# Kernel tuning notes

Measured on AMD Instinct MI355X. Metric: run time of the kernel, lower is better.

The kernel has to match this reference:

```python
import jax, jax.numpy as jnp
import numpy as np

# ---- static config (mirrors MonitorRetina init) ----
N, S, H, W = 256, 1, 144, 256        # stimulus: [N, S, H, W]
HR, WR = 144, 256                    # retina height/width
FOV_HALF_RAD = 0.5 * 75.0 * np.pi / 180.0   # Angular retina, degrees=75
GELU_GAMMA = 1.7015043497085571      # variance-preserving gain for gelu
OUT_OF_RANGE = 10.0                  # grid value for rays missing the monitor


def isotropic_grid_2d(h, w):
    """Pixel-center coordinates, isotropic (normalized by max dim), [-1,1] on the long axis."""
    m = float(max(h, w))
    y = (jnp.arange(h, dtype=jnp.float32) * 2.0 + 1.0 - h) / m
    x = (jnp.arange(w, dtype=jnp.float32) * 2.0 + 1.0 - w) / m
    gy, gx = jnp.meshgrid(y, x, indexing="ij")
    return gx, gy  # each [h, w]


def rmat_3d(ax, ay, az):
    """Batched 3D rotation matrix R = Rz @ Ry @ Rx from Euler angles, each [N]."""
    cx, sx = jnp.cos(ax), jnp.sin(ax)
    cy, sy = jnp.cos(ay), jnp.sin(ay)
    cz, sz = jnp.cos(az), jnp.sin(az)
    one, zero = jnp.ones_like(ax), jnp.zeros_like(ax)
    Rx = jnp.stack([one, zero, zero, zero, cx, -sx, zero, sx, cx], -1).reshape(-1, 3, 3)
    Ry = jnp.stack([cy, zero, sy, zero, one, zero, -sy, zero, cy], -1).reshape(-1, 3, 3)
    Rz = jnp.stack([cz, -sz, zero, sz, cz, zero, zero, zero, one], -1).reshape(-1, 3, 3)
    return jnp.einsum("nij,njk,nkl->nil", Rz, Ry, Rx)  # [N,3,3]


def retina_rays(rmat):
    """Angular retina: pixel angles -> unit ray directions, rotated per batch. [N,HR,WR,3]."""
    gx, gy = isotropic_grid_2d(HR, WR)
    ax, ay = gx * FOV_HALF_RAD, gy * FOV_HALF_RAD
    a = jnp.sqrt(ax * ax + ay * ay) + 1e-12
    sinc = jnp.sin(a) / a
    d = jnp.stack([sinc * ax, sinc * ay, jnp.cos(a)], -1)  # [HR,WR,3]
    return jnp.einsum("nij,hwj->nhwi", rmat, d)


def monitor_project(rays):
    """Plane monitor at unit distance along +z: perspective divide to isotropic grid coords. [N,HR,WR,2]."""
    rz = rays[..., 2]
    safe = rz > 1e-3
    inv = jnp.where(safe, rz, 1.0)
    gx = jnp.where(safe, rays[..., 0] / inv, OUT_OF_RANGE)
    gy = jnp.where(safe, rays[..., 1] / inv, OUT_OF_RANGE)
    return jnp.stack([gx, gy], -1)


def isotropic_grid_sample_2d(x, grid, pad_value=0.0):
    """Bilinear sample x:[N,C,H,W] at grid:[N,H',W',2] (isotropic coords), constant padding."""
    m = float(max(H, W))
    px = (grid[..., 0] * m + W - 1.0) * 0.5  # [N,H',W'] pixel coords
    py = (grid[..., 1] * m + H - 1.0) * 0.5
    x0 = jnp.floor(px)
    y0 = jnp.floor(py)
    wx = px - x0
    wy = py - y0
    x0i = x0.astype(jnp.int32)
    y0i = y0.astype(jnp.int32)

    def corner(img, yi, xi):
        valid = (xi >= 0) & (xi < W) & (yi >= 0) & (yi < H)
        v = img[:, jnp.clip(yi, 0, H - 1), jnp.clip(xi, 0, W - 1)]  # [C,H',W']
        return jnp.where(valid[None], v, pad_value)

    def one(img, y0i, x0i, wx, wy):
        v00 = corner(img, y0i, x0i)
        v01 = corner(img, y0i, x0i + 1)
        v10 = corner(img, y0i + 1, x0i)
        v11 = corner(img, y0i + 1, x0i + 1)
        return (v00 * (1 - wx) + v01 * wx) * (1 - wy) + (v10 * (1 - wx) + v11 * wx) * wy

    return jax.vmap(one)(x, y0i, x0i, wx, wy)  # [N,C,H',W']


def setup_inputs() -> dict:
    key = jax.random.key(0)
    ks = jax.random.split(key, 8)
    F, D = 16, 128
    return {
        "stimulus": jax.random.normal(ks[0], (N, S, H, W), jnp.float32),
        "perspective": jax.random.normal(ks[1], (N, F), jnp.float32),
        "W1": jax.random.normal(ks[2], (F, D), jnp.float32) / np.sqrt(F),
        "b1": jnp.zeros((D,), jnp.float32),
        "W2": jax.random.normal(ks[3], (D, D), jnp.float32) / np.sqrt(D),
        "b2": jnp.zeros((D,), jnp.float32),
        "Wp": jax.random.normal(ks[4], (D, 3), jnp.float32) * 0.05,  # proj gains init near 0
        "bp": jnp.zeros((3,), jnp.float32),
    }


def reference(stimulus, perspective, W1, b1, W2, b2, Wp, bp):
    # MLP -> 3 angles -> rotation matrix (rmat)
    h = jax.nn.gelu(perspective @ W1 + b1) * GELU_GAMMA
    h = jax.nn.gelu(h @ W2 + b2) * GELU_GAMMA
    ang = h @ Wp + bp                      # [N,3]
    rm = rmat_3d(ang[:, 0], ang[:, 1], ang[:, 2])
    rays = retina_rays(rm)                 # [N,HR,WR,3]
    grid = monitor_project(rays)           # [N,HR,WR,2]
    # monitor_pixel / retina_pixel are Raw (identity) transforms
    return isotropic_grid_sample_2d(stimulus, grid, pad_value=0.0)  # [N,S,HR,WR]
```

## Files before the change

### kernel.cpp

```cpp
#include <hip/hip_runtime.h>
#include <math.h>

#define NB    256
#define IMG_H 144
#define IMG_W 256
#define HR    144
#define WR    256
#define FDIM  16
#define DDIM  128

#define FOV_HALF_RAD 0.6544984694978736f
#define GELU_GAMMA   1.7015043497085571f
#define OUT_OF_RANGE 10.0f

__device__ __forceinline__ float gelu_gamma(float x) {
    const float k0 = 0.7978845608028654f;
    const float k1 = 0.044715f;
    float t = tanhf(k0 * (x + k1 * x * x * x));
    return 0.5f * x * (1.0f + t) * GELU_GAMMA;
}

__global__ void __launch_bounds__(DDIM) mlp_rmat_kernel(
    const float* __restrict__ persp,
    const float* __restrict__ W1,
    const float* __restrict__ b1,
    const float* __restrict__ W2,
    const float* __restrict__ b2,
    const float* __restrict__ Wp,
    const float* __restrict__ bp,
    float* __restrict__ Rout)
{
    const int n = blockIdx.x;
    const int d = threadIdx.x;

    __shared__ float sh1[DDIM];
    __shared__ float sh2[DDIM];
    __shared__ float ang[3];

    float acc = b1[d];
#pragma unroll
    for (int f = 0; f < FDIM; ++f)
        acc += persp[n * FDIM + f] * W1[f * DDIM + d];
    sh1[d] = gelu_gamma(acc);
    __syncthreads();

    float acc2 = b2[d];
#pragma unroll 8
    for (int k = 0; k < DDIM; ++k)
        acc2 += sh1[k] * W2[k * DDIM + d];
    sh2[d] = gelu_gamma(acc2);
    __syncthreads();

    if (d < 3) {
        float a = bp[d];
#pragma unroll 8
        for (int k = 0; k < DDIM; ++k)
            a += sh2[k] * Wp[k * 3 + d];
        ang[d] = a;
    }
    __syncthreads();

    if (d == 0) {
        float cx = cosf(ang[0]), sx = sinf(ang[0]);
        float cy = cosf(ang[1]), sy = sinf(ang[1]);
        float cz = cosf(ang[2]), sz = sinf(ang[2]);
        float* R = Rout + n * 9;
        R[0] = cz * cy;  R[1] = cz * sy * sx - sz * cx;  R[2] = cz * sy * cx + sz * sx;
        R[3] = sz * cy;  R[4] = sz * sy * sx + cz * cx;  R[5] = sz * sy * cx - cz * sx;
        R[6] = -sy;      R[7] = cy * sx;                 R[8] = cy * cx;
    }
}

__device__ __forceinline__ float fetch_px(const float* __restrict__ img, int yi, int xi) {
    bool valid = (xi >= 0) & (xi < IMG_W) & (yi >= 0) & (yi < IMG_H);
    return valid ? img[yi * IMG_W + xi] : 0.0f;
}

__global__ void __launch_bounds__(WR) retina_sample_kernel(
    const float* __restrict__ stim,
    const float* __restrict__ Rmat,
    float* __restrict__ out)
{
    const int w = threadIdx.x;
    const int h = blockIdx.x;
    const int n = blockIdx.y;

    const float* Rn = Rmat + n * 9;
    const float r0 = Rn[0], r1 = Rn[1], r2 = Rn[2];
    const float r3 = Rn[3], r4 = Rn[4], r5 = Rn[5];
    const float r6 = Rn[6], r7 = Rn[7], r8 = Rn[8];

    const float gx = (2.0f * w + 1.0f - 256.0f) * (1.0f / 256.0f);
    const float gy = (2.0f * h + 1.0f - 144.0f) * (1.0f / 256.0f);

    const float axv = gx * FOV_HALF_RAD;
    const float ayv = gy * FOV_HALF_RAD;
    const float t   = axv * axv + ayv * ayv;

    float sc = fmaf(t, 2.7557319e-6f, -1.9841270e-4f);
    sc = fmaf(t, sc,  8.3333333e-3f);
    sc = fmaf(t, sc, -1.6666667e-1f);
    sc = fmaf(t, sc,  1.0f);

    float ca = fmaf(t, 2.4801587e-5f, -1.3888889e-3f);
    ca = fmaf(t, ca,  4.1666667e-2f);
    ca = fmaf(t, ca, -0.5f);
    ca = fmaf(t, ca,  1.0f);

    const float dx = sc * axv, dy = sc * ayv, dz = ca;

    const float rx = r0 * dx + r1 * dy + r2 * dz;
    const float ry = r3 * dx + r4 * dy + r5 * dz;
    const float rz = r6 * dx + r7 * dy + r8 * dz;

    const float inv = __builtin_amdgcn_rcpf(rz);
    const bool safe = rz > 0.001f;
    const float gxp = safe ? rx * inv : OUT_OF_RANGE;
    const float gyp = safe ? ry * inv : OUT_OF_RANGE;

    const float px = fmaf(gxp, 256.0f, (float)(IMG_W - 1)) * 0.5f;
    const float py = fmaf(gyp, 256.0f, (float)(IMG_H - 1)) * 0.5f;

    const float x0f = floorf(px), y0f = floorf(py);
    const float wx = px - x0f, wy = py - y0f;
    const int x0 = (int)x0f, y0 = (int)y0f;

    const float* __restrict__ img = stim + (size_t)n * (IMG_H * IMG_W);
    const float v00 = fetch_px(img, y0,     x0);
    const float v01 = fetch_px(img, y0,     x0 + 1);
    const float v10 = fetch_px(img, y0 + 1, x0);
    const float v11 = fetch_px(img, y0 + 1, x0 + 1);

    const float top = v00 * (1.0f - wx) + v01 * wx;
    const float bot = v10 * (1.0f - wx) + v11 * wx;
    const float val = top * (1.0f - wy) + bot * wy;

    out[((size_t)n * HR + h) * WR + w] = val;
}

extern "C" void kernel_launch(void* const* d_in, const int* in_sizes, int n_in,
                              void* d_out, int out_size, void* d_ws, size_t ws_size,
                              hipStream_t stream) {
    const float* stimulus    = (const float*)d_in[0];
    const float* perspective = (const float*)d_in[1];
    const float* W1          = (const float*)d_in[2];
    const float* b1          = (const float*)d_in[3];
    const float* W2          = (const float*)d_in[4];
    const float* b2          = (const float*)d_in[5];
    const float* Wp          = (const float*)d_in[6];
    const float* bp          = (const float*)d_in[7];
    float* out = (float*)d_out;

    float* Rmat = (float*)d_ws;

    mlp_rmat_kernel<<<NB, DDIM, 0, stream>>>(
        perspective, W1, b1, W2, b2, Wp, bp, Rmat);

    dim3 grid(HR, NB);
    retina_sample_kernel<<<grid, WR, 0, stream>>>(stimulus, Rmat, out);
}
```

Before: 126.8 us.

## Compute four pixels per thread with vectorized nontemporal stores in retina sampler

Each thread now handles four adjacent output pixels instead of one, and each block covers four rows instead of one. All gather loads are issued together before the interpolation arithmetic, and results are written with a single 128-bit nontemporal store. The goal is more memory-level parallelism per thread, fewer blocks to schedule, fewer store instructions, and less cache pollution from the output stream. In exchange, each gather touches a wider spread of addresses per wavefront, register pressure goes up, and there are fewer threads overall.

```diff
diff --git a/kernel.cpp b/kernel.cpp
--- a/kernel.cpp
+++ b/kernel.cpp
@@ -12,6 +12,8 @@
 #define FOV_HALF_RAD 0.6544984694978736f
 #define GELU_GAMMA   1.7015043497085571f
 #define OUT_OF_RANGE 10.0f
+
+typedef float f32x4 __attribute__((ext_vector_type(4)));
 
 __device__ __forceinline__ float gelu_gamma(float x) {
     const float k0 = 0.7978845608028654f;
@@ -72,70 +74,88 @@
 }
 
 __device__ __forceinline__ float fetch_px(const float* __restrict__ img, int yi, int xi) {
-    bool valid = (xi >= 0) & (xi < IMG_W) & (yi >= 0) & (yi < IMG_H);
+    bool valid = ((unsigned)xi < IMG_W) & ((unsigned)yi < IMG_H);
     return valid ? img[yi * IMG_W + xi] : 0.0f;
 }
 
-__global__ void __launch_bounds__(WR) retina_sample_kernel(
+__global__ void __launch_bounds__(256) retina_sample_kernel(
     const float* __restrict__ stim,
     const float* __restrict__ Rmat,
     float* __restrict__ out)
 {
-    const int w = threadIdx.x;
-    const int h = blockIdx.x;
-    const int n = blockIdx.y;
+    const int tid = threadIdx.x;
+    const int n   = blockIdx.y;
+    const int h   = blockIdx.x * 4 + (tid >> 6);
+    const int w0  = (tid & 63) * 4;
 
     const float* Rn = Rmat + n * 9;
     const float r0 = Rn[0], r1 = Rn[1], r2 = Rn[2];
     const float r3 = Rn[3], r4 = Rn[4], r5 = Rn[5];
     const float r6 = Rn[6], r7 = Rn[7], r8 = Rn[8];
 
-    const float gx = (2.0f * w + 1.0f - 256.0f) * (1.0f / 256.0f);
-    const float gy = (2.0f * h + 1.0f - 144.0f) * (1.0f / 256.0f);
-
-    const float axv = gx * FOV_HALF_RAD;
+    const float gy  = (2.0f * h + 1.0f - 144.0f) * (1.0f / 256.0f);
     const float ayv = gy * FOV_HALF_RAD;
-    const float t   = axv * axv + ayv * ayv;
-
-    float sc = fmaf(t, 2.7557319e-6f, -1.9841270e-4f);
-    sc = fmaf(t, sc,  8.3333333e-3f);
-    sc = fmaf(t, sc, -1.6666667e-1f);
-    sc = fmaf(t, sc,  1.0f);
-
-    float ca = fmaf(t, 2.4801587e-5f, -1.3888889e-3f);
-    ca = fmaf(t, ca,  4.1666667e-2f);
-    ca = fmaf(t, ca, -0.5f);
-    ca = fmaf(t, ca,  1.0f);
-
-    const float dx = sc * axv, dy = sc * ayv, dz = ca;
-
-    const float rx = r0 * dx + r1 * dy + r2 * dz;
-    const float ry = r3 * dx + r4 * dy + r5 * dz;
-    const float rz = r6 * dx + r7 * dy + r8 * dz;
-
-    const float inv = __builtin_amdgcn_rcpf(rz);
-    const bool safe = rz > 0.001f;
-    const float gxp = safe ? rx * inv : OUT_OF_RANGE;
-    const float gyp = safe ? ry * inv : OUT_OF_RANGE;
-
-    const float px = fmaf(gxp, 256.0f, (float)(IMG_W - 1)) * 0.5f;
-    const float py = fmaf(gyp, 256.0f, (float)(IMG_H - 1)) * 0.5f;
-
-    const float x0f = floorf(px), y0f = floorf(py);
-    const float wx = px - x0f, wy = py - y0f;
-    const int x0 = (int)x0f, y0 = (int)y0f;
+    const float ay2 = ayv * ayv;
 
     const float* __restrict__ img = stim + (size_t)n * (IMG_H * IMG_W);
-    const float v00 = fetch_px(img, y0,     x0);
-    const float v01 = fetch_px(img, y0,     x0 + 1);
-    const float v10 = fetch_px(img, y0 + 1, x0);
-    const float v11 = fetch_px(img, y0 + 1, x0 + 1);
 
-    const float top = v00 * (1.0f - wx) + v01 * wx;
-    const float bot = v10 * (1.0f - wx) + v11 * wx;
-    const float val = top * (1.0f - wy) + bot * wy;
+    float px_[4], py_[4];
+    int   x0_[4], y0_[4];
+    float v00[4], v01[4], v10[4], v11[4];
 
-    out[((size_t)n * HR + h) * WR + w] = val;
+#pragma unroll
+    for (int j = 0; j < 4; ++j) {
+        const float gx  = (2.0f * (w0 + j) + 1.0f - 256.0f) * (1.0f / 256.0f);
+        const float axv = gx * FOV_HALF_RAD;
+        const float t   = axv * axv + ay2;
+
+        float sc = fmaf(t, 2.7557319e-6f, -1.9841270e-4f);
+        sc = fmaf(t, sc,  8.3333333e-3f);
+        sc = fmaf(t, sc, -1.6666667e-1f);
+        sc = fmaf(t, sc,  1.0f);
+
+        float ca = fmaf(t, 2.4801587e-5f, -1.3888889e-3f);
+        ca = fmaf(t, ca,  4.1666667e-2f);
+        ca = fmaf(t, ca, -0.5f);
+        ca = fmaf(t, ca,  1.0f);
+
+        const float dx = sc * axv, dy = sc * ayv, dz = ca;
+
+        const float rx = r0 * dx + r1 * dy + r2 * dz;
+        const float ry = r3 * dx + r4 * dy + r5 * dz;
+        const float rz = r6 * dx + r7 * dy + r8 * dz;
+
+        const float inv = __builtin_amdgcn_rcpf(rz);
+        const bool safe = rz > 0.001f;
+        const float gxp = safe ? rx * inv : OUT_OF_RANGE;
+        const float gyp = safe ? ry * inv : OUT_OF_RANGE;
+
+        px_[j] = fmaf(gxp, 256.0f, (float)(IMG_W - 1)) * 0.5f;
+        py_[j] = fmaf(gyp, 256.0f, (float)(IMG_H - 1)) * 0.5f;
+        x0_[j] = (int)floorf(px_[j]);
+        y0_[j] = (int)floorf(py_[j]);
+    }
+
+#pragma unroll
+    for (int j = 0; j < 4; ++j) {
+        v00[j] = fetch_px(img, y0_[j],     x0_[j]);
+        v01[j] = fetch_px(img, y0_[j],     x0_[j] + 1);
+        v10[j] = fetch_px(img, y0_[j] + 1, x0_[j]);
+        v11[j] = fetch_px(img, y0_[j] + 1, x0_[j] + 1);
+    }
+
+    f32x4 res;
+#pragma unroll
+    for (int j = 0; j < 4; ++j) {
+        const float wx = px_[j] - floorf(px_[j]);
+        const float wy = py_[j] - floorf(py_[j]);
+        const float top = v00[j] * (1.0f - wx) + v01[j] * wx;
+        const float bot = v10[j] * (1.0f - wx) + v11[j] * wx;
+        res[j] = top * (1.0f - wy) + bot * wy;
+    }
+
+    f32x4* dst = (f32x4*)(out + ((size_t)n * HR + h) * WR + w0);
+    __builtin_nontemporal_store(res, dst);
 }
 
 extern "C" void kernel_launch(void* const* d_in, const int* in_sizes, int n_in,
@@ -156,6 +176,6 @@
     mlp_rmat_kernel<<<NB, DDIM, 0, stream>>>(
         perspective, W1, b1, W2, b2, Wp, bp, Rmat);
 
-    dim3 grid(HR, NB);
-    retina_sample_kernel<<<grid, WR, 0, stream>>>(stimulus, Rmat, out);
+    dim3 grid(HR / 4, NB);
+    retina_sample_kernel<<<grid, 256, 0, stream>>>(stimulus, Rmat, out);
 }
```

After: 129.9 us. +2.4%, slower.

## Stage whole stimulus image in LDS per block and sample from shared memory

Applied to the files above, without the earlier changes.

Each block now handles one batch item. It copies the full 144x256 image into shared memory with vector loads, then each thread computes four output pixels and gathers their bilinear taps from LDS. Results go out as 128-bit nontemporal stores. This replaces scattered global gathers with LDS reads and reduces the block count. The trade-off is that one block per CU with a large LDS footprint leaves no overlap between the load phase and the compute phase.

```diff
diff --git a/kernel.cpp b/kernel.cpp
--- a/kernel.cpp
+++ b/kernel.cpp
@@ -4,6 +4,7 @@
 #define NB    256
 #define IMG_H 144
 #define IMG_W 256
+#define IMG_ELEMS (IMG_H * IMG_W)
 #define HR    144
 #define WR    256
 #define FDIM  16
@@ -12,6 +13,8 @@
 #define FOV_HALF_RAD 0.6544984694978736f
 #define GELU_GAMMA   1.7015043497085571f
 #define OUT_OF_RANGE 10.0f
+
+typedef float f32x4 __attribute__((ext_vector_type(4)));
 
 __device__ __forceinline__ float gelu_gamma(float x) {
     const float k0 = 0.7978845608028654f;
@@ -71,71 +74,105 @@
     }
 }
 
-__device__ __forceinline__ float fetch_px(const float* __restrict__ img, int yi, int xi) {
-    bool valid = (xi >= 0) & (xi < IMG_W) & (yi >= 0) & (yi < IMG_H);
-    return valid ? img[yi * IMG_W + xi] : 0.0f;
-}
-
-__global__ void __launch_bounds__(WR) retina_sample_kernel(
+__global__ void __launch_bounds__(1024, 1) retina_sample_kernel(
     const float* __restrict__ stim,
     const float* __restrict__ Rmat,
     float* __restrict__ out)
 {
-    const int w = threadIdx.x;
-    const int h = blockIdx.x;
-    const int n = blockIdx.y;
+    __shared__ float simg[IMG_ELEMS];
+
+    const int tid = threadIdx.x;
+    const int n   = blockIdx.x;
+
+    const float* __restrict__ img = stim + (size_t)n * IMG_ELEMS;
+
+    {
+        const f32x4* __restrict__ src = (const f32x4*)img;
+        f32x4* dstl = (f32x4*)simg;
+#pragma unroll
+        for (int p = 0; p < 9; ++p)
+            dstl[tid + p * 1024] = src[tid + p * 1024];
+    }
 
     const float* Rn = Rmat + n * 9;
     const float r0 = Rn[0], r1 = Rn[1], r2 = Rn[2];
     const float r3 = Rn[3], r4 = Rn[4], r5 = Rn[5];
     const float r6 = Rn[6], r7 = Rn[7], r8 = Rn[8];
 
-    const float gx = (2.0f * w + 1.0f - 256.0f) * (1.0f / 256.0f);
-    const float gy = (2.0f * h + 1.0f - 144.0f) * (1.0f / 256.0f);
+    __syncthreads();
 
-    const float axv = gx * FOV_HALF_RAD;
-    const float ayv = gy * FOV_HALF_RAD;
-    const float t   = axv * axv + ayv * ayv;
+#pragma unroll
+    for (int p = 0; p < 9; ++p) {
+        const int g   = tid + p * 1024;
+        const int px0 = g * 4;
+        const int h   = px0 >> 8;
+        const int w0  = px0 & 255;
 
-    float sc = fmaf(t, 2.7557319e-6f, -1.9841270e-4f);
-    sc = fmaf(t, sc,  8.3333333e-3f);
-    sc = fmaf(t, sc, -1.6666667e-1f);
-    sc = fmaf(t, sc,  1.0f);
+        const float gy  = (2.0f * h + 1.0f - 144.0f) * (1.0f / 256.0f);
+        const float ayv = gy * FOV_HALF_RAD;
+        const float ay2 = ayv * ayv;
 
-    float ca = fmaf(t, 2.4801587e-5f, -1.3888889e-3f);
-    ca = fmaf(t, ca,  4.1666667e-2f);
-    ca = fmaf(t, ca, -0.5f);
-    ca = fmaf(t, ca,  1.0f);
+        f32x4 res;
+#pragma unroll
+        for (int j = 0; j < 4; ++j) {
+            const float gx  = (2.0f * (w0 + j) + 1.0f - 256.0f) * (1.0f / 256.0f);
+            const float axv = gx * FOV_HALF_RAD;
+            const float t   = axv * axv + ay2;
 
-    const float dx = sc * axv, dy = sc * ayv, dz = ca;
+            float sc = fmaf(t, 2.7557319e-6f, -1.9841270e-4f);
+            sc = fmaf(t, sc,  8.3333333e-3f);
+            sc = fmaf(t, sc, -1.6666667e-1f);
+            sc = fmaf(t, sc,  1.0f);
 
-    const float rx = r0 * dx + r1 * dy + r2 * dz;
-    const float ry = r3 * dx + r4 * dy + r5 * dz;
-    const float rz = r6 * dx + r7 * dy + r8 * dz;
+            float ca = fmaf(t, 2.4801587e-5f, -1.3888889e-3f);
+            ca = fmaf(t, ca,  4.1666667e-2f);
+            ca = fmaf(t, ca, -0.5f);
+            ca = fmaf(t, ca,  1.0f);
 
-    const float inv = __builtin_amdgcn_rcpf(rz);
-    const bool safe = rz > 0.001f;
-    const float gxp = safe ? rx * inv : OUT_OF_RANGE;
-    const float gyp = safe ? ry * inv : OUT_OF_RANGE;
+            const float dx = sc * axv, dy = sc * ayv, dz = ca;
 
-    const float px = fmaf(gxp, 256.0f, (float)(IMG_W - 1)) * 0.5f;
-    const float py = fmaf(gyp, 256.0f, (float)(IMG_H - 1)) * 0.5f;
+            const float rx = r0 * dx + r1 * dy + r2 * dz;
+            const float ry = r3 * dx + r4 * dy + r5 * dz;
+            const float rz = r6 * dx + r7 * dy + r8 * dz;
 
-    const float x0f = floorf(px), y0f = floorf(py);
-    const float wx = px - x0f, wy = py - y0f;
-    const int x0 = (int)x0f, y0 = (int)y0f;
+            const float inv = __builtin_amdgcn_rcpf(rz);
+            const bool safe = rz > 0.001f;
+            const float gxp = safe ? rx * inv : OUT_OF_RANGE;
+            const float gyp = safe ? ry * inv : OUT_OF_RANGE;
 
-    const float* __restrict__ img = stim + (size_t)n * (IMG_H * IMG_W);
-    const float v00 = fetch_px(img, y0,     x0);
-    const float v01 = fetch_px(img, y0,     x0 + 1);
-    const float v10 = fetch_px(img, y0 + 1, x0);
-    const float v11 = fetch_px(img, y0 + 1, x0 + 1);
+            const float px = fmaf(gxp, 256.0f, (float)(IMG_W - 1)) * 0.5f;
+            const float py = fmaf(gyp, 256.0f, (float)(IMG_H - 1)) * 0.5f;
 
-    const float top = v00 * (1.0f - wx) + v01 * wx;
-    const float bot = v10 * (1.0f - wx) + v11 * wx;
-    const float val = top * (1.0f - wy) + bot * wy;
+            const float x0f = floorf(px), y0f = floorf(py);
+            const float wx = px - x0f, wy = py - y0f;
+            const int x0 = (int)x0f, y0 = (int)y0f;
+            const int x1 = x0 + 1,   y1 = y0 + 1;
 
-    out[((size_t)n * HR + h) * WR + w] = val;
+            const int xc0 = min(max(x0, 0), IMG_W - 1);
+            const int xc1 = min(max(x1, 0), IMG_W - 1);
+            const int yc0 = min(max(y0, 0), IMG_H - 1);
+            const int yc1 = min(max(y1, 0), IMG_H - 1);
+
+            const bool vx0 = (unsigned)x0 < IMG_W, vx1 = (unsigned)x1 < IMG_W;
+            const bool vy0 = (unsigned)y0 < IMG_H, vy1 = (unsigned)y1 < IMG_H;
+
+            float v00 = simg[yc0 * IMG_W + xc0];
+            float v01 = simg[yc0 * IMG_W + xc1];
+            float v10 = simg[yc1 * IMG_W + xc0];
+            float v11 = simg[yc1 * IMG_W + xc1];
+            v00 = (vx0 & vy0) ? v00 : 0.0f;
+            v01 = (vx1 & vy0) ? v01 : 0.0f;
+            v10 = (vx0 & vy1) ? v10 : 0.0f;
+            v11 = (vx1 & vy1) ? v11 : 0.0f;
+
+            const float top = v00 * (1.0f - wx) + v01 * wx;
+            const float bot = v10 * (1.0f - wx) + v11 * wx;
+            res[j] = top * (1.0f - wy) + bot * wy;
+        }
+
+        f32x4* dst = (f32x4*)(out + (size_t)n * IMG_ELEMS + px0);
+        __builtin_nontemporal_store(res, dst);
+    }
 }
 
 extern "C" void kernel_launch(void* const* d_in, const int* in_sizes, int n_in,
@@ -156,6 +193,5 @@
     mlp_rmat_kernel<<<NB, DDIM, 0, stream>>>(
         perspective, W1, b1, W2, b2, Wp, bp, Rmat);
 
-    dim3 grid(HR, NB);
-    retina_sample_kernel<<<grid, WR, 0, stream>>>(stimulus, Rmat, out);
+    retina_sample_kernel<<<NB, 1024, 0, stream>>>(stimulus, Rmat, out);
 }
```

After: 127.6 us. No clear change (+0.6%).
